# Kernel optimization log

Hardware: AMD Instinct MI355X
Metric: run time of the kernel (lower is better)

The kernel has to match this reference:

```python
import jax, jax.numpy as jnp
import numpy as np

B, S, E, H = 2, 2048, 1024, 16
D = E // H  # head_dim = 64


def setup_inputs() -> dict:
    key = jax.random.key(0)
    k1, k2, k3 = jax.random.split(key, 3)
    scale_in = 1.0 / np.sqrt(E)
    return {
        "x": jax.random.normal(k1, (B, S, E), dtype=jnp.float32),
        "W_attn": jax.random.normal(k2, (E, 3 * E), dtype=jnp.float32) * scale_in,
        "b_attn": jnp.zeros((3 * E,), dtype=jnp.float32),
        "W_proj": jax.random.normal(k3, (E, E), dtype=jnp.float32) * scale_in,
        "b_proj": jnp.zeros((E,), dtype=jnp.float32),
    }


def reference(x, W_attn, b_attn, W_proj, b_proj):
    # c_attn: fused QKV projection  [B,S,E] -> [B,S,3E]
    qkv = x @ W_attn + b_attn
    q, k, v = jnp.split(qkv, 3, axis=-1)
    # split heads -> [B,S,H,D]
    q = q.reshape(B, S, H, D)
    k = k.reshape(B, S, H, D)
    v = v.reshape(B, S, H, D)
    # scaled dot-product attention (no causal mask in the source module)
    scores = jnp.einsum("bqhd,bkhd->bhqk", q, k) / jnp.sqrt(jnp.float32(D))
    attn = jax.nn.softmax(scores, axis=-1)  # attn_dropout is identity in eval
    y = jnp.einsum("bhqk,bkhd->bqhd", attn, v).reshape(B, S, E)
    # c_proj; resid_dropout is identity in eval
    return y @ W_proj + b_proj
```

## Files before the change

kernel.cpp:

```cpp
#include <hip/hip_runtime.h>
#include <stdint.h>

#define NB 2
#define NS 2048
#define NE 1024
#define NH 16
#define ND 64
#define NE3 3072
#define NBS 4096
#define NT 32

typedef _Float16 half8 __attribute__((ext_vector_type(8)));
typedef __fp16 fp16x2 __attribute__((ext_vector_type(2)));
typedef float f32x4 __attribute__((ext_vector_type(4)));
typedef float f32x16 __attribute__((ext_vector_type(16)));
typedef unsigned int u32;

__device__ __forceinline__ void gload16(const void* g, void* l) {
  __builtin_amdgcn_global_load_lds(
      (__attribute__((address_space(1))) void*)const_cast<void*>(g),
      (__attribute__((address_space(3))) void*)l, 16, 0, 0);
}

__global__ void k_prep(const float* __restrict__ x, _Float16* __restrict__ xb,
                       const float* __restrict__ Wa, _Float16* __restrict__ WaT,
                       const float* __restrict__ Wp, _Float16* __restrict__ WpT) {
  int bid = blockIdx.x;
  int t = threadIdx.x;
  if (bid < 2048) {
    int i = bid * 256 + t;
    const float4* s = (const float4*)x + (size_t)i * 2;
    float4 a = s[0], b = s[1];
    half8 o;
    o[0]=(_Float16)a.x; o[1]=(_Float16)a.y; o[2]=(_Float16)a.z; o[3]=(_Float16)a.w;
    o[4]=(_Float16)b.x; o[5]=(_Float16)b.y; o[6]=(_Float16)b.z; o[7]=(_Float16)b.w;
    *((half8*)xb + i) = o;
    return;
  }
  __shared__ _Float16 tile[64][72];
  int bb = bid - 2048;
  int bx = bb >> 4, ky = bb & 15;
  const float* src; _Float16* dst; int N;
  if (bx < 48) { src = Wa; dst = WaT; N = NE3; }
  else         { src = Wp; dst = WpT; N = NE; bx -= 48; }
  const int K = NE;
  int n0 = bx * 64, k0 = ky * 64;
  int kk = t >> 2, nc = (t & 3) << 4;
  const float* sp = src + (size_t)(k0 + kk) * N + n0 + nc;
#pragma unroll
  for (int j = 0; j < 16; j += 4) {
    float4 v = *(const float4*)(sp + j);
    tile[kk][nc + j + 0] = (_Float16)v.x;
    tile[kk][nc + j + 1] = (_Float16)v.y;
    tile[kk][nc + j + 2] = (_Float16)v.z;
    tile[kk][nc + j + 3] = (_Float16)v.w;
  }
  __syncthreads();
  int nn = t >> 2, kc = (t & 3) << 4;
  half8 o0, o1;
#pragma unroll
  for (int j = 0; j < 8; ++j) { o0[j] = tile[kc + j][nn]; o1[j] = tile[kc + 8 + j][nn]; }
  _Float16* op = dst + (size_t)(n0 + nn) * K + k0 + kc;
  *(half8*)op = o0;
  *(half8*)(op + 8) = o1;
}

template <int OUT_HALF, int BM>
__global__ __launch_bounds__(256, 2)
void k_gemm(const _Float16* __restrict__ A, const _Float16* __restrict__ Bt,
            const float* __restrict__ bias, void* __restrict__ Cv,
            int M, int N, int K) {
  constexpr int ACH = BM / 16;
  constexpr int CHUNKS = ACH + 8;
  constexpr int PER_WAVE = CHUNKS / 4;
  constexpr int JN = (BM == 128) ? 4 : 2;
  __shared__ _Float16 As[2][BM * 32];
  __shared__ _Float16 Bs[2][128 * 32];
  const int nwg = gridDim.x * gridDim.y;
  const int d = blockIdx.y * gridDim.x + blockIdx.x;
  const int lid = (d & 7) * (nwg >> 3) + (d >> 3);
  const int bx = lid % gridDim.x, by = lid / gridDim.x;
  const int m0 = by * BM, n0 = bx * 128;
  const int t = threadIdx.x, l = t & 63, w = t >> 6;
  const int wr = (BM == 128) ? (w >> 1) : 0;
  const int wc = (BM == 128) ? (w & 1) : w;
  const int srow = l >> 2;
  const int sk = (l & 3) << 3;
  f32x4 acc[4][JN] = {};

#define G_STAGE(KT, BUF)                                                              \
  {                                                                                   \
    _Pragma("unroll")                                                                 \
    for (int p = 0; p < PER_WAVE; ++p) {                                              \
      int cid = w * PER_WAVE + p;                                                     \
      if (cid < ACH)                                                                  \
        gload16(A + (size_t)(m0 + cid * 16 + srow) * K + (KT) * 32 + sk,              \
                (char*)&As[BUF][0] + cid * 1024);                                     \
      else                                                                            \
        gload16(Bt + (size_t)(n0 + (cid - ACH) * 16 + srow) * K + (KT) * 32 + sk,     \
                (char*)&Bs[BUF][0] + (cid - ACH) * 1024);                             \
    }                                                                                 \
  }

  const int T = K / 32;
  G_STAGE(0, 0);
  G_STAGE(1, 1);
  for (int tt = 0; tt < T; ++tt) {
    if (tt + 1 < T) {
      if constexpr (PER_WAVE == 4) asm volatile("s_waitcnt vmcnt(4)" ::: "memory");
      else                         asm volatile("s_waitcnt vmcnt(3)" ::: "memory");
    } else {
      asm volatile("s_waitcnt vmcnt(0)" ::: "memory");
    }
    __builtin_amdgcn_s_barrier();
    asm volatile("" ::: "memory");
    const int cur = tt & 1;
    const _Float16* as = &As[cur][0];
    const _Float16* bs = &Bs[cur][0];
    half8 a[4], b[JN];
#pragma unroll
    for (int i = 0; i < 4; ++i)
      a[i] = *(const half8*)(as + (wr * 64 + i * 16 + (l & 15)) * 32 + ((l >> 4) << 3));
#pragma unroll
    for (int j = 0; j < JN; ++j)
      b[j] = *(const half8*)(bs + ((BM == 128 ? wc * 64 : wc * 32) + j * 16 + (l & 15)) * 32 + ((l >> 4) << 3));
#pragma unroll
    for (int i = 0; i < 4; ++i)
#pragma unroll
      for (int j = 0; j < JN; ++j)
        acc[i][j] = __builtin_amdgcn_mfma_f32_16x16x32_f16(a[i], b[j], acc[i][j], 0, 0, 0);
    asm volatile("s_waitcnt lgkmcnt(0)" ::: "memory");
    __builtin_amdgcn_s_barrier();
    asm volatile("" ::: "memory");
    if (tt + 2 < T) G_STAGE(tt + 2, cur);
  }
#undef G_STAGE

  float bv[JN];
#pragma unroll
  for (int j = 0; j < JN; ++j)
    bv[j] = bias[n0 + (BM == 128 ? wc * 64 : wc * 32) + j * 16 + (l & 15)];
#pragma unroll
  for (int i = 0; i < 4; ++i) {
    int row0 = m0 + wr * 64 + i * 16 + ((l >> 4) << 2);
#pragma unroll
    for (int j = 0; j < JN; ++j) {
      int col = n0 + (BM == 128 ? wc * 64 : wc * 32) + j * 16 + (l & 15);
#pragma unroll
      for (int r = 0; r < 4; ++r) {
        float v = acc[i][j][r] + bv[j];
        if (OUT_HALF) {
          if (col < NE) v *= 0.18033688011112042f;
          ((_Float16*)Cv)[(size_t)(row0 + r) * N + col] = (_Float16)v;
        } else {
          ((float*)Cv)[(size_t)(row0 + r) * N + col] = v;
        }
      }
    }
  }
}

__global__ void k_vt(const _Float16* __restrict__ qkv, _Float16* __restrict__ Vt) {
  __shared__ _Float16 tile[64][72];
  int s0 = blockIdx.x * 64;
  int bh = blockIdx.y, b = bh >> 4, h = bh & 15;
  int t = threadIdx.x;
  int ss = t >> 2, dc = (t & 3) << 4;
  const _Float16* sp = qkv + (size_t)(b * NS + s0 + ss) * NE3 + 2 * NE + h * ND + dc;
  half8 v0 = *(const half8*)sp, v1 = *(const half8*)(sp + 8);
#pragma unroll
  for (int j = 0; j < 8; ++j) { tile[ss][dc + j] = v0[j]; tile[ss][dc + 8 + j] = v1[j]; }
  __syncthreads();
  int d = t >> 2, sc = (t & 3) << 4;
  half8 o0, o1;
#pragma unroll
  for (int j = 0; j < 8; ++j) { o0[j] = tile[sc + j][d]; o1[j] = tile[sc + 8 + j][d]; }
  _Float16* op = Vt + (size_t)(bh * ND + d) * NS + s0 + sc;
  *(half8*)op = o0;
  *(half8*)(op + 8) = o1;
}

__global__ __launch_bounds__(256, 2)
void k_attn(const _Float16* __restrict__ qkv, const _Float16* __restrict__ Vt,
            _Float16* __restrict__ Y) {
  __shared__ _Float16 Kb[2][64 * 64];
  __shared__ _Float16 Vb[2][64 * 64];
  const int dly = blockIdx.y * gridDim.x + blockIdx.x;
  const int lid = (dly & 7) * 64 + (dly >> 3);
  const int bh = lid >> 4, qb = lid & 15;
  const int q0 = qb * 128;
  const int b = bh >> 4, h = bh & 15;
  const int t = threadIdx.x, l = t & 63, w = t >> 6;
  const int c = l & 31, hh = l >> 5;

  half8 qf[4];
  {
    const _Float16* qp = qkv + (size_t)(b * NS + q0 + w * 32 + c) * NE3 + h * ND + 8 * hh;
    qf[0] = *(const half8*)(qp);
    qf[1] = *(const half8*)(qp + 16);
    qf[2] = *(const half8*)(qp + 32);
    qf[3] = *(const half8*)(qp + 48);
  }

  f32x16 Oa0 = {}, Oa1 = {}, Osum = {};
  f32x16 saE0, saE1, saO0, saO1;
  half8 ones;
#pragma unroll
  for (int j = 0; j < 8; ++j) ones[j] = (_Float16)1.0f;

  const int lh4 = l >> 4;
  const int ls7 = (l >> 1) & 7;
  const int l1 = l & 1;
  const int grp = c >> 1;
  const int xr = grp & 7;

#define RD_BASE (grp * 256 + ((c & 1) << 4))

#define STAGE_K(KT, BUF)                                                             \
  {                                                                                  \
    _Pragma("unroll")                                                                \
    for (int i = 0; i < 2; ++i) {                                                    \
      int ci = w * 2 + i;                                                            \
      int g = 4 * ci + lh4;                                                          \
      int row = 2 * g + l1;                                                          \
      int j8 = (ls7 ^ (g & 7)) << 3;                                                 \
      gload16(qkv + (size_t)(b * NS + (KT) * 64 + row) * NE3 + NE + h * ND + j8,     \
              (char*)&Kb[BUF][0] + ci * 1024);                                       \
    }                                                                                \
  }
#define STAGE_V(KT, BUF)                                                             \
  {                                                                                  \
    _Pragma("unroll")                                                                \
    for (int i = 0; i < 2; ++i) {                                                    \
      int ci = w * 2 + i;                                                            \
      int g = 4 * ci + lh4;                                                          \
      int row = 2 * g + l1;                                                          \
      int j8 = (ls7 ^ (g & 7)) << 3;                                                 \
      gload16(Vt + (size_t)(bh * ND + row) * NS + (KT) * 64 + j8,                    \
              (char*)&Vb[BUF][0] + ci * 1024);                                       \
    }                                                                                \
  }

#define QK_TILE(BUF, SA0, SA1)                                                       \
  {                                                                                  \
    SA0 = (f32x16){}; SA1 = (f32x16){};                                              \
    _Pragma("unroll")                                                                \
    for (int tt = 0; tt < 4; ++tt) {                                                 \
      int off = RD_BASE + (((2 * tt + hh) ^ xr) << 5);                               \
      half8 kf0 = *(const half8*)((char*)&Kb[BUF][0] + off);                         \
      half8 kf1 = *(const half8*)((char*)&Kb[BUF][0] + off + 4096);                  \
      SA0 = __builtin_amdgcn_mfma_f32_32x32x16_f16(kf0, qf[tt], SA0, 0, 0, 0);       \
      SA1 = __builtin_amdgcn_mfma_f32_32x32x16_f16(kf1, qf[tt], SA1, 0, 0, 0);       \
    }                                                                                \
  }

#define PVSTEP(KK, DARR, CUR)                                                         \
    {                                                                                 \
      u32 pb0 = DARR[2 * ((KK) & 1)][0], pa0 = DARR[2 * ((KK) & 1) + 1][0];           \
      u32 pb1 = DARR[2 * ((KK) & 1)][1], pa1 = DARR[2 * ((KK) & 1) + 1][1];           \
      u32 sent0 = hh ? pb0 : pa0;                                                     \
      u32 sent1 = hh ? pb1 : pa1;                                                     \
      u32 recv0 = __shfl_xor(sent0, 32);                                              \
      u32 recv1 = __shfl_xor(sent1, 32);                                              \
      union { u32 d[4]; half8 h; } pfu;                                               \
      pfu.d[0] = hh ? recv0 : pb0;                                                    \
      pfu.d[1] = hh ? recv1 : pb1;                                                    \
      pfu.d[2] = hh ? pa0 : recv0;                                                    \
      pfu.d[3] = hh ? pa1 : recv1;                                                    \
      int offv = RD_BASE + (((2 * (KK) + hh) ^ xr) << 5);                             \
      half8 vf0 = *(const half8*)((char*)&Vb[CUR][0] + offv);                         \
      half8 vf1 = *(const half8*)((char*)&Vb[CUR][0] + offv + 4096);                  \
      Oa0 = __builtin_amdgcn_mfma_f32_32x32x16_f16(pfu.h, vf0, Oa0, 0, 0, 0);         \
      Oa1 = __builtin_amdgcn_mfma_f32_32x32x16_f16(pfu.h, vf1, Oa1, 0, 0, 0);         \
      Osum = __builtin_amdgcn_mfma_f32_32x32x16_f16(pfu.h, ones, Osum, 0, 0, 0);      \
    }

#define TILE_BODY(T, CUR, SAC0, SAC1, SAN0, SAN1)                                     \
  {                                                                                   \
    u32 D0[4][2], D1[4][2];                                                           \
    _Pragma("unroll")                                                                 \
    for (int s = 0; s < 4; ++s) {                                                     \
      fp16x2 e0 = __builtin_amdgcn_cvt_pkrtz(__builtin_amdgcn_exp2f(SAC0[4 * s + 0]), \
                                             __builtin_amdgcn_exp2f(SAC0[4 * s + 1]));\
      fp16x2 e1 = __builtin_amdgcn_cvt_pkrtz(__builtin_amdgcn_exp2f(SAC0[4 * s + 2]), \
                                             __builtin_amdgcn_exp2f(SAC0[4 * s + 3]));\
      fp16x2 e2 = __builtin_amdgcn_cvt_pkrtz(__builtin_amdgcn_exp2f(SAC1[4 * s + 0]), \
                                             __builtin_amdgcn_exp2f(SAC1[4 * s + 1]));\
      fp16x2 e3 = __builtin_amdgcn_cvt_pkrtz(__builtin_amdgcn_exp2f(SAC1[4 * s + 2]), \
                                             __builtin_amdgcn_exp2f(SAC1[4 * s + 3]));\
      D0[s][0] = __builtin_bit_cast(u32, e0);                                         \
      D0[s][1] = __builtin_bit_cast(u32, e1);                                         \
      D1[s][0] = __builtin_bit_cast(u32, e2);                                         \
      D1[s][1] = __builtin_bit_cast(u32, e3);                                         \
    }                                                                                 \
    if ((T) + 1 < NT) QK_TILE((CUR) ^ 1, SAN0, SAN1);                                 \
    PVSTEP(0, D0, CUR)                                                                \
    PVSTEP(1, D0, CUR)                                                                \
    PVSTEP(2, D1, CUR)                                                                \
    PVSTEP(3, D1, CUR)                                                                \
    __syncthreads();                                                                  \
    if ((T) + 2 < NT) STAGE_V((T) + 2, CUR);                                          \
    if ((T) + 3 < NT) STAGE_K((T) + 3, (CUR) ^ 1);                                    \
  }

  STAGE_K(0, 0);
  STAGE_V(0, 0);
  STAGE_K(1, 1);
  __syncthreads();
  QK_TILE(0, saE0, saE1);
  __syncthreads();
  STAGE_V(1, 1);
  STAGE_K(2, 0);

  for (int kt = 0; kt < NT; kt += 2) {
    TILE_BODY(kt, 0, saE0, saE1, saO0, saO1);
    TILE_BODY(kt + 1, 1, saO0, saO1, saE0, saE1);
  }
#undef TILE_BODY
#undef PVSTEP
#undef QK_TILE
#undef STAGE_K
#undef STAGE_V
#undef RD_BASE

#pragma unroll
  for (int i = 0; i < 16; ++i) {
    int ql = (i & 3) + 8 * (i >> 2) + 4 * hh;
    float inv = 1.0f / Osum[i];
    size_t base = (size_t)(b * NS + q0 + w * 32 + ql) * NE + h * ND + c;
    Y[base] = (_Float16)(Oa0[i] * inv);
    Y[base + 32] = (_Float16)(Oa1[i] * inv);
  }
}

extern "C" void kernel_launch(void* const* d_in, const int* in_sizes, int n_in,
                              void* d_out, int out_size, void* d_ws, size_t ws_size,
                              hipStream_t stream) {
  (void)in_sizes; (void)n_in; (void)out_size; (void)ws_size;
  const float* x      = (const float*)d_in[0];
  const float* W_attn = (const float*)d_in[1];
  const float* b_attn = (const float*)d_in[2];
  const float* W_proj = (const float*)d_in[3];
  const float* b_proj = (const float*)d_in[4];
  char* ws = (char*)d_ws;
  const size_t MB = 1024 * 1024;
  _Float16* qkvb = (_Float16*)(ws);
  _Float16* WaT  = (_Float16*)(ws + 24 * MB);
  _Float16* WpT  = (_Float16*)(ws + 30 * MB);
  _Float16* xb   = (_Float16*)(ws + 32 * MB);
  _Float16* Vt   = (_Float16*)(ws + 40 * MB);
  _Float16* yb   = (_Float16*)(ws + 32 * MB);

  k_prep<<<dim3(2048 + 1024), dim3(256), 0, stream>>>(x, xb, W_attn, WaT, W_proj, WpT);
  k_gemm<1, 128><<<dim3(NE3 / 128, NBS / 128), dim3(256), 0, stream>>>(xb, WaT, b_attn, (void*)qkvb, NBS, NE3, NE);
  k_vt<<<dim3(NS / 64, NB * NH), dim3(256), 0, stream>>>(qkvb, Vt);
  k_attn<<<dim3(NS / 128, NB * NH), dim3(256), 0, stream>>>(qkvb, Vt, yb);
  k_gemm<0, 64><<<dim3(NE / 128, NBS / 64), dim3(256), 0, stream>>>(yb, WpT, b_proj, d_out, NBS, NE, NE);
}
```

Baseline: 122.8 us.

## Replace QKV projection GEMM with 256x256-tile 8-wave pipelined kernel

Adds a dedicated QKV GEMM that uses 512 threads and 256x256 output tiles with a BK=64 double-buffered LDS pipeline. Tiles arrive through direct global-to-LDS loads into an XOR-swizzled layout, and the A and B staging are split around two barriers so loads overlap the MFMA work. The epilogue folds the Q scaling constant (about 1/sqrt(64) times log2 e) into the Q columns, which the attention kernel must already expect. The larger tile means more reuse per block, but it launches only 192 blocks and needs more registers and LDS per block, which may lower occupancy.

After: 130.1 us. 1.06x slower.

```diff
diff --git a/kernel.cpp b/kernel.cpp
--- a/kernel.cpp
+++ b/kernel.cpp
@@ -63,6 +63,136 @@
   _Float16* op = dst + (size_t)(n0 + nn) * K + k0 + kc;
   *(half8*)op = o0;
   *(half8*)(op + 8) = o1;
+}
+
+__global__ __launch_bounds__(512)
+void k_gemm8(const _Float16* __restrict__ A, const _Float16* __restrict__ Bt,
+             const float* __restrict__ bias, _Float16* __restrict__ C) {
+  __shared__ _Float16 As[2][2][128 * 64];
+  __shared__ _Float16 Bs[2][2][128 * 64];
+  const int nwg = 12 * 16;
+  const int d = blockIdx.y * 12 + blockIdx.x;
+  const int lid = (d & 7) * (nwg >> 3) + (d >> 3);
+  const int bx = lid % 12, by = lid / 12;
+  const int m0 = by * 256, n0 = bx * 256;
+  const int t = threadIdx.x, l = t & 63, w = t >> 6;
+  const int wr = w >> 2, wc = w & 3;
+  const int lh4 = l >> 4, ls7 = (l >> 1) & 7, l1 = l & 1;
+  const int aw = (w & 3) * 4;
+  const int bh = (w >> 1) & 1;
+  const int bw = ((w & 1) | ((w >> 2) << 1)) * 4;
+  f32x4 acc[8][4] = {};
+
+#define STAGE_A8(KT, BUF)                                                             \
+  {                                                                                   \
+    _Pragma("unroll")                                                                 \
+    for (int i = 0; i < 4; ++i) {                                                     \
+      int ci = aw + i;                                                                \
+      int r = 8 * ci + 2 * lh4 + l1;                                                  \
+      int j8 = (ls7 ^ ((4 * ci + lh4) & 7)) << 3;                                     \
+      gload16(A + (size_t)(m0 + wr * 128 + r) * 1024 + (KT) * 64 + j8,                \
+              (char*)&As[BUF][wr][0] + ci * 1024);                                    \
+    }                                                                                 \
+  }
+#define STAGE_B8(KT, BUF)                                                             \
+  {                                                                                   \
+    _Pragma("unroll")                                                                 \
+    for (int i = 0; i < 4; ++i) {                                                     \
+      int ci = bw + i;                                                                \
+      int r = 8 * ci + 2 * lh4 + l1;                                                  \
+      int j8 = (ls7 ^ ((4 * ci + lh4) & 7)) << 3;                                     \
+      gload16(Bt + (size_t)(n0 + bh * 128 + r) * 1024 + (KT) * 64 + j8,               \
+              (char*)&Bs[BUF][bh][0] + ci * 1024);                                    \
+    }                                                                                 \
+  }
+#define PIADDR(BASE, RL, J) \
+  ((char*)(BASE) + ((RL) >> 1) * 256 + ((((J) ^ (((RL) >> 1) & 7))) << 5) + (((RL) & 1) << 4))
+
+  STAGE_B8(0, 0);
+  STAGE_A8(0, 0);
+  STAGE_B8(1, 1);
+
+  for (int tt = 0; tt < 16; ++tt) {
+    const int buf = tt & 1;
+    if (tt < 15) asm volatile("s_waitcnt vmcnt(4) lgkmcnt(0)" ::: "memory");
+    else         asm volatile("s_waitcnt vmcnt(0) lgkmcnt(0)" ::: "memory");
+    __builtin_amdgcn_s_barrier();
+    asm volatile("" ::: "memory");
+    if (tt + 1 < 16) STAGE_A8(tt + 1, (tt + 1) & 1);
+    half8 bf[4][2];
+#pragma unroll
+    for (int n = 0; n < 4; ++n)
+#pragma unroll
+      for (int ks = 0; ks < 2; ++ks) {
+        int rbl = (wc & 1) * 64 + n * 16 + (l & 15);
+        bf[n][ks] = *(const half8*)PIADDR(&Bs[buf][bh][0], rbl, ks * 4 + lh4);
+      }
+    {
+      half8 af[2][2];
+#pragma unroll
+      for (int s = 0; s < 2; ++s)
+#pragma unroll
+        for (int ks = 0; ks < 2; ++ks) {
+          int ral = s * 16 + (l & 15);
+          af[s][ks] = *(const half8*)PIADDR(&As[buf][wr][0], ral, ks * 4 + lh4);
+        }
+      __builtin_amdgcn_s_setprio(1);
+#pragma unroll
+      for (int s = 0; s < 2; ++s)
+#pragma unroll
+        for (int n = 0; n < 4; ++n)
+#pragma unroll
+          for (int ks = 0; ks < 2; ++ks)
+            acc[s][n] = __builtin_amdgcn_mfma_f32_16x16x32_f16(af[s][ks], bf[n][ks], acc[s][n], 0, 0, 0);
+      __builtin_amdgcn_s_setprio(0);
+    }
+    asm volatile("s_waitcnt lgkmcnt(0)" ::: "memory");
+    __builtin_amdgcn_s_barrier();
+    asm volatile("" ::: "memory");
+    if (tt + 2 < 16) STAGE_B8(tt + 2, buf);
+#pragma unroll
+    for (int q = 1; q < 4; ++q) {
+      half8 af[2][2];
+#pragma unroll
+      for (int s = 0; s < 2; ++s)
+#pragma unroll
+        for (int ks = 0; ks < 2; ++ks) {
+          int ral = q * 32 + s * 16 + (l & 15);
+          af[s][ks] = *(const half8*)PIADDR(&As[buf][wr][0], ral, ks * 4 + lh4);
+        }
+      __builtin_amdgcn_s_setprio(1);
+#pragma unroll
+      for (int s = 0; s < 2; ++s)
+#pragma unroll
+        for (int n = 0; n < 4; ++n)
+#pragma unroll
+          for (int ks = 0; ks < 2; ++ks)
+            acc[2 * q + s][n] = __builtin_amdgcn_mfma_f32_16x16x32_f16(af[s][ks], bf[n][ks], acc[2 * q + s][n], 0, 0, 0);
+      __builtin_amdgcn_s_setprio(0);
+    }
+  }
+#undef STAGE_A8
+#undef STAGE_B8
+#undef PIADDR
+
+  float bv[4];
+#pragma unroll
+  for (int n = 0; n < 4; ++n) bv[n] = bias[n0 + wc * 64 + n * 16 + (l & 15)];
+#pragma unroll
+  for (int m = 0; m < 8; ++m) {
+    int row0 = m0 + wr * 128 + m * 16 + lh4 * 4;
+#pragma unroll
+    for (int n = 0; n < 4; ++n) {
+      int col = n0 + wc * 64 + n * 16 + (l & 15);
+      float scale = (col < NE) ? 0.18033688011112042f : 1.0f;
+#pragma unroll
+      for (int r = 0; r < 4; ++r) {
+        float v = (acc[m][n][r] + bv[n]) * ((col < NE) ? 1.0f : 1.0f);
+        v = (acc[m][n][r] + bv[n]) * scale;
+        C[(size_t)(row0 + r) * NE3 + col] = (_Float16)v;
+      }
+    }
+  }
 }
 
 template <int OUT_HALF, int BM>
@@ -352,7 +482,7 @@
   _Float16* yb   = (_Float16*)(ws + 32 * MB);
 
   k_prep<<<dim3(2048 + 1024), dim3(256), 0, stream>>>(x, xb, W_attn, WaT, W_proj, WpT);
-  k_gemm<1, 128><<<dim3(NE3 / 128, NBS / 128), dim3(256), 0, stream>>>(xb, WaT, b_attn, (void*)qkvb, NBS, NE3, NE);
+  k_gemm8<<<dim3(12, 16), dim3(512), 0, stream>>>(xb, WaT, b_attn, qkvb);
   k_vt<<<dim3(NS / 64, NB * NH), dim3(256), 0, stream>>>(qkvb, Vt);
   k_attn<<<dim3(NS / 128, NB * NH), dim3(256), 0, stream>>>(qkvb, Vt, yb);
   k_gemm<0, 64><<<dim3(NE / 128, NBS / 64), dim3(256), 0, stream>>>(yb, WpT, b_proj, d_out, NBS, NE, NE);
```
